# Kernel tuning notes

Measured on AMD Instinct MI355X. Metric: run time of the kernel, lower is better.

The kernel has to match this reference:

```python
import jax, jax.numpy as jnp
import numpy as np

D_MODEL = 2048
N_HEADS = 16
D_K = D_MODEL // N_HEADS
THETA = 10000.0
BATCH = 4
SEQ = 2048


def apply_rope(x, positions, theta=THETA):
    # x: [b, h, s, d], positions: [b, s]
    d = x.shape[-1]
    inv_freq = theta ** (-jnp.arange(0, d, 2, dtype=jnp.float32) / d)  # [d/2]
    ang = positions.astype(jnp.float32)[:, None, :, None] * inv_freq  # [b,1,s,d/2]
    cos, sin = jnp.cos(ang), jnp.sin(ang)
    x1, x2 = x[..., 0::2], x[..., 1::2]
    rot = jnp.stack([x1 * cos - x2 * sin, x1 * sin + x2 * cos], axis=-1)
    return rot.reshape(x.shape).astype(x.dtype)


def setup_inputs() -> dict:
    key = jax.random.key(0)
    ks = jax.random.split(key, 5)
    scale = 1.0 / np.sqrt(D_MODEL)
    return {
        "x": jax.random.normal(ks[0], (BATCH, SEQ, D_MODEL), dtype=jnp.float32),
        "Wq": jax.random.normal(ks[1], (D_MODEL, D_MODEL), dtype=jnp.float32) * scale,
        "Wk": jax.random.normal(ks[2], (D_MODEL, D_MODEL), dtype=jnp.float32) * scale,
        "Wv": jax.random.normal(ks[3], (D_MODEL, D_MODEL), dtype=jnp.float32) * scale,
        "Wo": jax.random.normal(ks[4], (D_MODEL, D_MODEL), dtype=jnp.float32) * scale,
        "token_positions": jnp.broadcast_to(jnp.arange(SEQ, dtype=jnp.int32), (BATCH, SEQ)),
    }


def reference(x, Wq, Wk, Wv, Wo, token_positions):
    b, s, _ = x.shape
    # Linear layers use y = x @ W.T (weight [out, in], no bias)
    q = jnp.einsum('bsd,ed->bse', x, Wq).reshape(b, s, N_HEADS, D_K).transpose(0, 2, 1, 3)
    k = jnp.einsum('bsd,ed->bse', x, Wk).reshape(b, s, N_HEADS, D_K).transpose(0, 2, 1, 3)
    v = jnp.einsum('bsd,ed->bse', x, Wv).reshape(b, s, N_HEADS, D_K).transpose(0, 2, 1, 3)
    q = apply_rope(q, token_positions)
    k = apply_rope(k, token_positions)
    scores = jnp.einsum('bhqd,bhkd->bhqk', q, k) / jnp.sqrt(jnp.float32(D_K))
    causal = jnp.tril(jnp.ones((s, s), dtype=bool))
    scores = jnp.where(causal[None, None], scores, jnp.finfo(scores.dtype).min)
    attn = jax.nn.softmax(scores, axis=-1)
    out = jnp.einsum('bhqk,bhkd->bhqd', attn, v)  # [b,h,s,d]
    out = out.transpose(0, 2, 1, 3).reshape(b, s, D_MODEL)
    return jnp.einsum('bsd,ed->bse', out, Wo)
```

## Files before the change

kernel.cpp:

```cpp
#include <hip/hip_runtime.h>

typedef unsigned int   u32;
typedef unsigned short u16;
typedef float f32x4  __attribute__((ext_vector_type(4)));
typedef float f32x16 __attribute__((ext_vector_type(16)));
typedef short s16x8  __attribute__((ext_vector_type(8)));
typedef u16   u16x4  __attribute__((ext_vector_type(4)));
typedef u16   u16x8  __attribute__((ext_vector_type(8)));
typedef u32   u32x4  __attribute__((ext_vector_type(4)));

#define DEVI __device__ __forceinline__

DEVI u16 f2bf(float f) {
  u32 u = __builtin_bit_cast(u32, f);
  u = (u + 0x7fffu + ((u >> 16) & 1u)) >> 16;
  return (u16)u;
}
DEVI float bf2f(u16 h) { u32 u = (u32)h << 16; return __builtin_bit_cast(float, u); }

DEVI void gload_lds16(const void* g, void* l) {
  __builtin_amdgcn_global_load_lds(
      (const __attribute__((address_space(1))) void*)g,
      (__attribute__((address_space(3))) void*)l, 16, 0, 0);
}

__global__ __launch_bounds__(256)
void convert_kernel(const float* __restrict__ x, const float* __restrict__ Wq,
                    const float* __restrict__ Wk, const float* __restrict__ Wv,
                    const float* __restrict__ Wo, u16* __restrict__ xb, u16* __restrict__ Wb)
{
  const int NX = 1 << 21;
  const int NT = NX + (1 << 21);
  for (int idx = blockIdx.x * 256 + threadIdx.x; idx < NT; idx += gridDim.x * 256) {
    const float* src; u16* dst; size_t off;
    if (idx < NX) { src = x; dst = xb; off = (size_t)idx * 8; }
    else {
      int i2 = idx - NX;
      int wsel = i2 >> 19, r = i2 & ((1 << 19) - 1);
      src = (wsel == 0) ? Wq : (wsel == 1) ? Wk : (wsel == 2) ? Wv : Wo;
      dst = Wb + (size_t)wsel * 4194304;
      off = (size_t)r * 8;
    }
    float4 a = *(const float4*)(src + off), b = *(const float4*)(src + off + 4);
    u16x8 o;
    o[0] = f2bf(a.x); o[1] = f2bf(a.y); o[2] = f2bf(a.z); o[3] = f2bf(a.w);
    o[4] = f2bf(b.x); o[5] = f2bf(b.y); o[6] = f2bf(b.z); o[7] = f2bf(b.w);
    *(u16x8*)(dst + off) = o;
  }
}

template<int EPI, int NBX>
__global__ __launch_bounds__(512, 2)
void gemm256(const u16* __restrict__ Ab, const u16* __restrict__ Bb,
             u16* __restrict__ Qh, u16* __restrict__ Kh, u16* __restrict__ Vt,
             float* __restrict__ Of)
{
  constexpr int K  = 2048;
  constexpr int NTILE = K / 64;
  constexpr int GX = NBX / 4;
  __shared__ __attribute__((aligned(16))) char smem[131072];

  const int t = threadIdx.x;
  const int lane = t & 63, w = t >> 6;
  const int lo = lane & 15, hi = lane >> 4;
  const int wr = w >> 2, wc = w & 3;

  const int nwg = gridDim.x;
  const int cpx = nwg >> 3;
  const int sbid = (blockIdx.x & 7) * cpx + (blockIdx.x >> 3);
  const int g = sbid >> 4, l = sbid & 15;
  const int bx = (g % GX) * 4 + (l & 3);
  const int by = (g / GX) * 4 + (l >> 2);
  const int m0 = by * 256, n0 = bx * 256;

  auto stage = [&](const u16* gbase, char* lds) {
#pragma unroll
    for (int j = 0; j < 4; ++j) {
      int chunk = j * 512 + w * 64 + lane;
      int row = chunk >> 3, cc = chunk & 7;
      const u16* g2 = gbase + (size_t)row * K + ((cc ^ (row & 7)) * 8);
      gload_lds16(g2, lds + (size_t)(j * 512 + w * 64) * 16);
    }
  };

  f32x4 zero = {0.f, 0.f, 0.f, 0.f};
  f32x4 acc[8][4];
#pragma unroll
  for (int i = 0; i < 8; ++i)
#pragma unroll
    for (int j = 0; j < 4; ++j) acc[i][j] = zero;

  const u16* Abase = Ab + (size_t)m0 * K;
  const u16* Bbase = Bb + (size_t)n0 * K;

  stage(Abase + 0 * 64, smem);
  stage(Bbase + 0 * 64, smem + 32768);
  stage(Abase + 1 * 64, smem + 65536);
  stage(Bbase + 1 * 64, smem + 65536 + 32768);

  for (int tt = 0; tt < NTILE; ++tt) {
    if (tt < NTILE - 1) {
      asm volatile("s_waitcnt vmcnt(8)\n\ts_barrier" ::: "memory");
    } else {
      asm volatile("s_waitcnt vmcnt(0)\n\ts_barrier" ::: "memory");
    }
    const char* Alp = smem + (size_t)(tt & 1) * 65536;
    const char* Blp = Alp + 32768;

    s16x8 af0[8], bf0[4];
#pragma unroll
    for (int i = 0; i < 8; ++i) {
      int ra = wr * 128 + i * 16 + lo;
      af0[i] = *(const s16x8*)(Alp + ra * 128 + ((hi * 16) ^ ((ra & 7) << 4)));
    }
#pragma unroll
    for (int j = 0; j < 4; ++j) {
      int rb = wc * 64 + j * 16 + lo;
      bf0[j] = *(const s16x8*)(Blp + rb * 128 + ((hi * 16) ^ ((rb & 7) << 4)));
    }
    __builtin_amdgcn_s_setprio(1);
#pragma unroll
    for (int i = 0; i < 8; ++i)
#pragma unroll
      for (int j = 0; j < 4; ++j)
        acc[i][j] = __builtin_amdgcn_mfma_f32_16x16x32_bf16(af0[i], bf0[j], acc[i][j], 0, 0, 0);
    __builtin_amdgcn_s_setprio(0);

    s16x8 af1[8], bf1[4];
#pragma unroll
    for (int i = 0; i < 8; ++i) {
      int ra = wr * 128 + i * 16 + lo;
      af1[i] = *(const s16x8*)(Alp + ra * 128 + (((4 + hi) * 16) ^ ((ra & 7) << 4)));
    }
#pragma unroll
    for (int j = 0; j < 4; ++j) {
      int rb = wc * 64 + j * 16 + lo;
      bf1[j] = *(const s16x8*)(Blp + rb * 128 + (((4 + hi) * 16) ^ ((rb & 7) << 4)));
    }
    asm volatile("s_waitcnt lgkmcnt(0)\n\ts_barrier" ::: "memory");
    if (tt + 2 < NTILE) {
      char* dst = smem + (size_t)(tt & 1) * 65536;
      stage(Abase + (tt + 2) * 64, dst);
      stage(Bbase + (tt + 2) * 64, dst + 32768);
    }
    __builtin_amdgcn_s_setprio(1);
#pragma unroll
    for (int i = 0; i < 8; ++i)
#pragma unroll
      for (int j = 0; j < 4; ++j)
        acc[i][j] = __builtin_amdgcn_mfma_f32_16x16x32_bf16(af1[i], bf1[j], acc[i][j], 0, 0, 0);
    __builtin_amdgcn_s_setprio(0);
  }

  const int mb = m0 + wr * 128;
  const int nb = n0 + wc * 64;
  if (EPI == 0) {
    const int wsel = n0 >> 11;
    u16* Out = (wsel == 0) ? Qh : (wsel == 1) ? Kh : Vt;
#pragma unroll
    for (int i = 0; i < 8; ++i) {
      int m = mb + i * 16 + hi * 4;
      int b = m >> 11, s0 = m & 2047;
#pragma unroll
      for (int j = 0; j < 4; ++j) {
        int nn = (nb + j * 16 + lo) & 2047;
        int h = nn >> 7, d = nn & 127;
        if (wsel < 2) {
#pragma unroll
          for (int r = 0; r < 4; ++r)
            Out[((size_t)((b * 16 + h) * 2048) + s0 + r) * 128 + d] = f2bf(acc[i][j][r]);
        } else {
          u16x4 v;
#pragma unroll
          for (int r = 0; r < 4; ++r) v[r] = f2bf(acc[i][j][r]);
          *(u16x4*)(Out + ((size_t)(b * 16 + h) * 128 + d) * 2048 + s0) = v;
        }
      }
    }
  } else {
#pragma unroll
    for (int i = 0; i < 8; ++i)
#pragma unroll
      for (int j = 0; j < 4; ++j) {
        int n = nb + j * 16 + lo;
#pragma unroll
        for (int r = 0; r < 4; ++r)
          Of[(size_t)(mb + i * 16 + hi * 4 + r) * 2048 + n] = acc[i][j][r];
      }
  }
}

template<int AM, int WM, int EPI>
__global__ __launch_bounds__(256, 2)
void gemm_nt(const void* __restrict__ Ap, const void* __restrict__ Wp, void* __restrict__ Cp)
{
  constexpr int K = 2048;
  __shared__ __attribute__((aligned(16))) u16 Al[128 * 64];
  __shared__ __attribute__((aligned(16))) u16 Bl[128 * 64];

  const int t = threadIdx.x;
  const int lane = t & 63, w = t >> 6;
  const int lo = lane & 15, hi = lane >> 4;
  const int wm = w >> 1, wn = w & 1;
  const int m0 = blockIdx.y * 128, n0 = blockIdx.x * 128;

  f32x4 zero = {0.f, 0.f, 0.f, 0.f};
  f32x4 acc[4][4];
#pragma unroll
  for (int i = 0; i < 4; ++i)
#pragma unroll
    for (int j = 0; j < 4; ++j) acc[i][j] = zero;

  for (int k0 = 0; k0 < K; k0 += 64) {
    __syncthreads();
    if (AM == 1) {
      const u16* A = (const u16*)Ap;
#pragma unroll
      for (int j = 0; j < 4; ++j) {
        int row = (w * 4 + j) * 8 + (lane >> 3);
        const u16* g = A + (size_t)(m0 + row) * K + k0 + (lane & 7) * 8;
        gload_lds16(g, (char*)Al + (w * 4 + j) * 1024);
      }
    } else {
      const float* A = (const float*)Ap;
#pragma unroll
      for (int c = 0; c < 2; ++c) {
        int chunk = c * 256 + t;
        int row = chunk >> 2, q = chunk & 3;
        const float4* g = reinterpret_cast<const float4*>(A + (size_t)(m0 + row) * K + k0 + q * 16);
        float4 v0 = g[0], v1 = g[1], v2 = g[2], v3 = g[3];
        u16x8 o0, o1;
        o0[0] = f2bf(v0.x); o0[1] = f2bf(v0.y); o0[2] = f2bf(v0.z); o0[3] = f2bf(v0.w);
        o0[4] = f2bf(v1.x); o0[5] = f2bf(v1.y); o0[6] = f2bf(v1.z); o0[7] = f2bf(v1.w);
        o1[0] = f2bf(v2.x); o1[1] = f2bf(v2.y); o1[2] = f2bf(v2.z); o1[3] = f2bf(v2.w);
        o1[4] = f2bf(v3.x); o1[5] = f2bf(v3.y); o1[6] = f2bf(v3.z); o1[7] = f2bf(v3.w);
        int swz = (row & 7) << 4;
        char* base = (char*)Al + row * 128;
        *(u16x8*)(base + ((q * 32)      ^ swz)) = o0;
        *(u16x8*)(base + ((q * 32 + 16) ^ swz)) = o1;
      }
    }
    if (WM == 1) {
      const u16* B = (const u16*)Wp;
#pragma unroll
      for (int j = 0; j < 4; ++j) {
        int row = (w * 4 + j) * 8 + (lane >> 3);
        const u16* g = B + (size_t)(n0 + row) * K + k0 + (lane & 7) * 8;
        gload_lds16(g, (char*)Bl + (w * 4 + j) * 1024);
      }
    } else {
      const float* B = (const float*)Wp;
#pragma unroll
      for (int c = 0; c < 2; ++c) {
        int chunk = c * 256 + t;
        int row = chunk >> 2, q = chunk & 3;
        const float4* g = reinterpret_cast<const float4*>(B + (size_t)(n0 + row) * K + k0 + q * 16);
        float4 v0 = g[0], v1 = g[1], v2 = g[2], v3 = g[3];
        u16x8 o0, o1;
        o0[0] = f2bf(v0.x); o0[1] = f2bf(v0.y); o0[2] = f2bf(v0.z); o0[3] = f2bf(v0.w);
        o0[4] = f2bf(v1.x); o0[5] = f2bf(v1.y); o0[6] = f2bf(v1.z); o0[7] = f2bf(v1.w);
        o1[0] = f2bf(v2.x); o1[1] = f2bf(v2.y); o1[2] = f2bf(v2.z); o1[3] = f2bf(v2.w);
        o1[4] = f2bf(v3.x); o1[5] = f2bf(v3.y); o1[6] = f2bf(v3.z); o1[7] = f2bf(v3.w);
        int swz = (row & 7) << 4;
        char* base = (char*)Bl + row * 128;
        *(u16x8*)(base + ((q * 32)      ^ swz)) = o0;
        *(u16x8*)(base + ((q * 32 + 16) ^ swz)) = o1;
      }
    }
    __syncthreads();
#pragma unroll
    for (int kk = 0; kk < 2; ++kk) {
      s16x8 af[4], bfr[4];
#pragma unroll
      for (int i = 0; i < 4; ++i) {
        int ra = wm * 64 + i * 16 + lo;
        int ca = (kk * 4 + hi) * 16; if (AM != 1) ca ^= (ra & 7) << 4;
        af[i]  = *(const s16x8*)((const char*)Al + ra * 128 + ca);
        int rb = wn * 64 + i * 16 + lo;
        int cb = (kk * 4 + hi) * 16; if (WM != 1) cb ^= (rb & 7) << 4;
        bfr[i] = *(const s16x8*)((const char*)Bl + rb * 128 + cb);
      }
#pragma unroll
      for (int i = 0; i < 4; ++i)
#pragma unroll
        for (int j = 0; j < 4; ++j)
          acc[i][j] = __builtin_amdgcn_mfma_f32_16x16x32_bf16(af[i], bfr[j], acc[i][j], 0, 0, 0);
    }
  }

  const int mb = m0 + wm * 64, nb = n0 + wn * 64;
  if (EPI == 0) {
    u16* Out = (u16*)Cp;
#pragma unroll
    for (int i = 0; i < 4; ++i)
#pragma unroll
      for (int j = 0; j < 4; ++j) {
        int n = nb + j * 16 + lo;
        int h = n >> 7, d = n & 127;
#pragma unroll
        for (int r = 0; r < 4; ++r) {
          int m = mb + i * 16 + hi * 4 + r;
          int b = m >> 11, s = m & 2047;
          Out[((size_t)((b * 16 + h) * 2048 + s)) * 128 + d] = f2bf(acc[i][j][r]);
        }
      }
  } else if (EPI == 1) {
    u16* Out = (u16*)Cp;
#pragma unroll
    for (int i = 0; i < 4; ++i)
#pragma unroll
      for (int j = 0; j < 4; ++j) {
        int n = nb + j * 16 + lo;
        int h = n >> 7, d = n & 127;
        int m = mb + i * 16 + hi * 4;
        int b = m >> 11, s = m & 2047;
        u16x4 v;
#pragma unroll
        for (int r = 0; r < 4; ++r) v[r] = f2bf(acc[i][j][r]);
        *(u16x4*)(Out + ((size_t)((b * 16 + h) * 128 + d)) * 2048 + s) = v;
      }
  } else {
    float* Out = (float*)Cp;
#pragma unroll
    for (int i = 0; i < 4; ++i)
#pragma unroll
      for (int j = 0; j < 4; ++j) {
        int n = nb + j * 16 + lo;
#pragma unroll
        for (int r = 0; r < 4; ++r) {
          int m = mb + i * 16 + hi * 4 + r;
          Out[(size_t)m * 2048 + n] = acc[i][j][r];
        }
      }
  }
}

__global__ __launch_bounds__(256)
void rope_k_kernel(u16* __restrict__ Kh, const int* __restrict__ pos)
{
  const int NP = 4 * 16 * 2048 * 64;
  const float C = -0.20762050593046014f;
  for (int idx = blockIdx.x * 256 + threadIdx.x; idx < NP; idx += gridDim.x * 256) {
    int i = idx & 63;
    int srow = idx >> 6;
    int s = srow & 2047;
    int b = srow >> 15;
    int p = pos[(b << 11) + s];
    float ang = (float)p * exp2f(C * (float)i);
    float sn, cs;
    sincosf(ang, &sn, &cs);
    u32* kp = (u32*)Kh + (size_t)srow * 64 + i;
    u32 v = *kp;
    float x1 = bf2f((u16)(v & 0xffffu)), x2 = bf2f((u16)(v >> 16));
    *kp = (u32)f2bf(x1 * cs - x2 * sn) | ((u32)f2bf(x1 * sn + x2 * cs) << 16);
  }
}

__global__ __launch_bounds__(256, 2)
void attn_kernel(const u16* __restrict__ Qh, const u16* __restrict__ Kh,
                 const u16* __restrict__ Vt, const int* __restrict__ pos,
                 u16* __restrict__ AO)
{
  __shared__ __attribute__((aligned(16))) char smem[65536];

  const int t = threadIdx.x, lane = t & 63, w = t >> 6;
  const int q5 = lane & 31, h5 = lane >> 5;
  const int bid = blockIdx.x;
  const int bh = (((bid >> 3) & 7) << 3) | (bid & 7);
  const int qt = bid >> 6;
  const int qbase = (15 - qt) * 128;
  const int b = bh >> 4;
  const int qrow0 = qbase + w * 32;
  const int q_abs = qrow0 + q5;

  const u16* Kb = Kh + (size_t)bh * 2048 * 128;
  const u16* Vb = Vt + (size_t)bh * 128 * 2048;

  auto stageKV = [&](int kv0, char* dst) {
#pragma unroll
    for (int j = 0; j < 4; ++j) {
      int chunk = j * 256 + w * 64 + lane;
      int row = chunk >> 4, cc = chunk & 15;
      const u16* g = Kb + (size_t)(kv0 + row) * 128 + ((cc ^ (row & 15)) * 8);
      gload_lds16(g, dst + (size_t)chunk * 16);
    }
#pragma unroll
    for (int j = 0; j < 4; ++j) {
      int chunk = j * 256 + w * 64 + lane;
      int pr = chunk >> 4, o16 = chunk & 15;
      int orig = o16 ^ (pr & 15);
      int grow = ((orig >> 3) << 6) + pr;
      const u16* g = Vb + (size_t)grow * 2048 + kv0 + ((orig & 7) * 8);
      gload_lds16(g, dst + 16384 + (size_t)chunk * 16);
    }
  };

  s16x8 qb[8];
  const float CF = -0.20762050593046014f;
  const float QSCALE = 0.08838834764831845f * 1.4426950408889634f;
  {
    float p = (float)pos[(b << 11) + q_abs];
    const u16* qrow = Qh + ((size_t)bh * 2048 + q_abs) * 128;
#pragma unroll
    for (int kb = 0; kb < 8; ++kb) {
      s16x8 raw = *reinterpret_cast<const s16x8*>(qrow + kb * 16 + h5 * 8);
      s16x8 out;
#pragma unroll
      for (int u = 0; u < 4; ++u) {
        float x1 = bf2f((u16)raw[2 * u]), x2 = bf2f((u16)raw[2 * u + 1]);
        float ang = p * exp2f(CF * (float)(kb * 8 + h5 * 4 + u));
        float sn, cs; sincosf(ang, &sn, &cs);
        sn *= QSCALE; cs *= QSCALE;
        out[2 * u]     = (short)f2bf(x1 * cs - x2 * sn);
        out[2 * u + 1] = (short)f2bf(x1 * sn + x2 * cs);
      }
      qb[kb] = out;
    }
  }

  f32x16 o[4];
#pragma unroll
  for (int d = 0; d < 4; ++d)
#pragma unroll
    for (int r = 0; r < 16; ++r) o[d][r] = 0.f;
  float m2 = -1e30f, lp = 0.f;

  const int ntiles = (qbase + 128) >> 6;

  stageKV(0, smem);
  if (ntiles > 1) stageKV(64, smem + 32768);

  for (int tile = 0; tile < ntiles; ++tile) {
    const int kv0 = tile << 6;
    if (tile < ntiles - 1) {
      asm volatile("s_waitcnt vmcnt(8)\n\ts_barrier" ::: "memory");
    } else {
      asm volatile("s_waitcnt vmcnt(0)\n\ts_barrier" ::: "memory");
    }
    const char* Kl = smem + (size_t)(tile & 1) * 32768;
    const char* Vl = Kl + 16384;

    f32x16 st[2];
#pragma unroll
    for (int tt = 0; tt < 2; ++tt)
#pragma unroll
      for (int r = 0; r < 16; ++r) st[tt][r] = 0.f;
    __builtin_amdgcn_s_setprio(1);
#pragma unroll
    for (int tt = 0; tt < 2; ++tt) {
      const char* krow = Kl + (tt * 32 + q5) * 256;
      const int swz = (q5 & 15) << 4;
#pragma unroll
      for (int kb = 0; kb < 8; ++kb) {
        s16x8 ka = *(const s16x8*)(krow + ((kb * 32 + h5 * 16) ^ swz));
        st[tt] = __builtin_amdgcn_mfma_f32_32x32x16_bf16(ka, qb[kb], st[tt], 0, 0, 0);
      }
    }
    __builtin_amdgcn_s_setprio(0);

    const bool needmask = (kv0 + 63 > qrow0);
    float pm = -1e30f;
    if (needmask) {
#pragma unroll
      for (int tt = 0; tt < 2; ++tt)
#pragma unroll
        for (int r = 0; r < 16; ++r) {
          int kvloc = (r & 3) + 8 * (r >> 2) + 4 * h5 + 32 * tt;
          float v = st[tt][r];
          if (kv0 + kvloc > q_abs) v = -1e30f;
          st[tt][r] = v;
          pm = fmaxf(pm, v);
        }
    } else {
#pragma unroll
      for (int tt = 0; tt < 2; ++tt)
#pragma unroll
        for (int r = 0; r < 16; ++r) pm = fmaxf(pm, st[tt][r]);
    }

    if (__any(pm - m2 > 8.0f)) {
      float tm = fmaxf(pm, __shfl_xor(pm, 32));
      float mn = fmaxf(m2, tm);
      float alpha = exp2f(m2 - mn);
      m2 = mn; lp *= alpha;
#pragma unroll
      for (int d = 0; d < 4; ++d)
#pragma unroll
        for (int r = 0; r < 16; ++r) o[d][r] *= alpha;
    }

    s16x8 pb[2][2];
#pragma unroll
    for (int tt = 0; tt < 2; ++tt) {
      u32 pk[8], sw[8];
      float acc = 0.f;
#pragma unroll
      for (int i = 0; i < 8; ++i) {
        float e0 = exp2f(st[tt][2 * i]     - m2);
        float e1 = exp2f(st[tt][2 * i + 1] - m2);
        acc += e0 + e1;
        pk[i] = (u32)f2bf(e0) | ((u32)f2bf(e1) << 16);
      }
      lp += acc;
#pragma unroll
      for (int i = 0; i < 8; ++i)
        sw[i] = (u32)__shfl_xor((int)pk[i], 32);
#pragma unroll
      for (int kv2 = 0; kv2 < 2; ++kv2) {
        int i0 = kv2 * 4;
        u32x4 tmp;
        tmp[0] = h5 ? sw[i0 + 2] : pk[i0];
        tmp[1] = h5 ? sw[i0 + 3] : pk[i0 + 1];
        tmp[2] = h5 ? pk[i0 + 2] : sw[i0];
        tmp[3] = h5 ? pk[i0 + 3] : sw[i0 + 1];
        pb[tt][kv2] = __builtin_bit_cast(s16x8, tmp);
      }
    }

    __builtin_amdgcn_s_setprio(1);
#pragma unroll
    for (int d = 0; d < 4; ++d) {
      const char* vrow = Vl + (((d & 1) * 32 + q5) * 256);
      const int vbase = (d >> 1) * 128;
      const int swz = (q5 & 15) << 4;
#pragma unroll
      for (int tt = 0; tt < 2; ++tt)
#pragma unroll
        for (int kv2 = 0; kv2 < 2; ++kv2) {
          s16x8 va = *(const s16x8*)(vrow + ((vbase + tt * 64 + kv2 * 32 + h5 * 16) ^ swz));
          o[d] = __builtin_amdgcn_mfma_f32_32x32x16_bf16(va, pb[tt][kv2], o[d], 0, 0, 0);
        }
    }
    __builtin_amdgcn_s_setprio(0);

    asm volatile("s_waitcnt lgkmcnt(0)\n\ts_barrier" ::: "memory");
    if (tile + 2 < ntiles)
      stageKV((tile + 2) * 64, smem + (size_t)(tile & 1) * 32768);
  }

  float lt = lp + __shfl_xor(lp, 32);
  float inv = 1.0f / lt;
  __syncthreads();
  char* Olw = smem + w * 8192;
#pragma unroll
  for (int d4 = 0; d4 < 4; ++d4)
#pragma unroll
    for (int r = 0; r < 16; ++r) {
      int dd = d4 * 32 + (r & 3) + 8 * (r >> 2) + 4 * h5;
      *(u16*)(Olw + q5 * 256 + ((dd * 2) ^ ((q5 & 7) << 4))) = f2bf(o[d4][r] * inv);
    }
  __syncthreads();
  const int h = bh & 15;
#pragma unroll
  for (int c = 0; c < 8; ++c) {
    int chunk = c * 256 + t;
    int row = chunk >> 4, sl = chunk & 15;
    u16x8 v = *(const u16x8*)(smem + row * 256 + ((sl * 16) ^ ((row & 7) << 4)));
    *(u16x8*)(AO + ((size_t)(b * 2048 + qbase + row)) * 2048 + h * 128 + sl * 8) = v;
  }
}

extern "C" void kernel_launch(void* const* d_in, const int* in_sizes, int n_in,
                              void* d_out, int out_size, void* d_ws, size_t ws_size,
                              hipStream_t stream)
{
  const float* x  = (const float*)d_in[0];
  const float* Wq = (const float*)d_in[1];
  const float* Wk = (const float*)d_in[2];
  const float* Wv = (const float*)d_in[3];
  const float* Wo = (const float*)d_in[4];
  const int*  pos = (const int*)d_in[5];

  char* ws = (char*)d_ws;
  const size_t MB32 = 33554432;
  u16* Qh = (u16*)(ws);
  u16* Kh = (u16*)(ws + MB32);
  u16* Vt = (u16*)(ws + 2 * MB32);

  dim3 blk(256);

  if (ws_size >= (size_t)167772160) {
    u16* xb = (u16*)(ws + 3 * MB32);
    u16* Wb = (u16*)(ws + 4 * MB32);
    u16* AO = xb;
    convert_kernel<<<2048, blk, 0, stream>>>(x, Wq, Wk, Wv, Wo, xb, Wb);
    gemm256<0, 24><<<768, 512, 0, stream>>>(xb, Wb, Qh, Kh, Vt, nullptr);
    rope_k_kernel<<<2048, blk, 0, stream>>>(Kh, pos);
    attn_kernel<<<1024, blk, 0, stream>>>(Qh, Kh, Vt, pos, AO);
    gemm256<1, 8><<<256, 512, 0, stream>>>(AO, Wb + 3 * 4194304, nullptr, nullptr, nullptr,
                                           (float*)d_out);
  } else {
    u16* AO = (u16*)(ws + 3 * MB32);
    dim3 gg(16, 64);
    gemm_nt<0, 0, 0><<<gg, blk, 0, stream>>>(x, Wq, Qh);
    gemm_nt<0, 0, 0><<<gg, blk, 0, stream>>>(x, Wk, Kh);
    gemm_nt<0, 0, 1><<<gg, blk, 0, stream>>>(x, Wv, Vt);
    rope_k_kernel<<<2048, blk, 0, stream>>>(Kh, pos);
    attn_kernel<<<1024, blk, 0, stream>>>(Qh, Kh, Vt, pos, AO);
    gemm_nt<1, 0, 2><<<gg, blk, 0, stream>>>(AO, Wo, d_out);
  }
}
```

Measured before the change: 440.0 us.

## Fuse K RoPE into QKV GEMM epilogue and remap tile groups

```diff
diff --git a/kernel.cpp b/kernel.cpp
--- a/kernel.cpp
+++ b/kernel.cpp
@@ -53,11 +53,10 @@
 __global__ __launch_bounds__(512, 2)
 void gemm256(const u16* __restrict__ Ab, const u16* __restrict__ Bb,
              u16* __restrict__ Qh, u16* __restrict__ Kh, u16* __restrict__ Vt,
-             float* __restrict__ Of)
+             float* __restrict__ Of, const int* __restrict__ pos)
 {
   constexpr int K  = 2048;
   constexpr int NTILE = K / 64;
-  constexpr int GX = NBX / 4;
   __shared__ __attribute__((aligned(16))) char smem[131072];
 
   const int t = threadIdx.x;
@@ -69,8 +68,17 @@
   const int cpx = nwg >> 3;
   const int sbid = (blockIdx.x & 7) * cpx + (blockIdx.x >> 3);
   const int g = sbid >> 4, l = sbid & 15;
-  const int bx = (g % GX) * 4 + (l & 3);
-  const int by = (g / GX) * 4 + (l >> 2);
+  int gx, gy;
+  if (NBX == 24) {
+    int c3 = g % 3, c2 = (g / 3) & 1, cm = g / 6;
+    gx = (cm & 1) * 3 + c3;
+    gy = (cm >> 1) * 2 + c2;
+  } else {
+    gx = g % (NBX / 4);
+    gy = g / (NBX / 4);
+  }
+  const int bx = gx * 4 + (l & 3);
+  const int by = gy * 4 + (l >> 2);
   const int m0 = by * 256, n0 = bx * 256;
 
   auto stage = [&](const u16* gbase, char* lds) {
@@ -157,6 +165,7 @@
   if (EPI == 0) {
     const int wsel = n0 >> 11;
     u16* Out = (wsel == 0) ? Qh : (wsel == 1) ? Kh : Vt;
+    const float CF = -0.20762050593046014f;
 #pragma unroll
     for (int i = 0; i < 8; ++i) {
       int m = mb + i * 16 + hi * 4;
@@ -165,10 +174,22 @@
       for (int j = 0; j < 4; ++j) {
         int nn = (nb + j * 16 + lo) & 2047;
         int h = nn >> 7, d = nn & 127;
-        if (wsel < 2) {
+        if (wsel == 0) {
 #pragma unroll
           for (int r = 0; r < 4; ++r)
             Out[((size_t)((b * 16 + h) * 2048) + s0 + r) * 128 + d] = f2bf(acc[i][j][r]);
+        } else if (wsel == 1) {
+          float fr = exp2f(CF * (float)(d >> 1));
+#pragma unroll
+          for (int r = 0; r < 4; ++r) {
+            float own = acc[i][j][r];
+            float oth = __shfl_xor(own, 1, 64);
+            float p = (float)pos[(b << 11) + s0 + r];
+            float ang = p * fr;
+            float cs = __cosf(ang), sn = __sinf(ang);
+            float v = (lo & 1) ? (oth * sn + own * cs) : (own * cs - oth * sn);
+            Out[((size_t)((b * 16 + h) * 2048) + s0 + r) * 128 + d] = f2bf(v);
+          }
         } else {
           u16x4 v;
 #pragma unroll
@@ -584,11 +605,10 @@
     u16* Wb = (u16*)(ws + 4 * MB32);
     u16* AO = xb;
     convert_kernel<<<2048, blk, 0, stream>>>(x, Wq, Wk, Wv, Wo, xb, Wb);
-    gemm256<0, 24><<<768, 512, 0, stream>>>(xb, Wb, Qh, Kh, Vt, nullptr);
-    rope_k_kernel<<<2048, blk, 0, stream>>>(Kh, pos);
+    gemm256<0, 24><<<768, 512, 0, stream>>>(xb, Wb, Qh, Kh, Vt, nullptr, pos);
     attn_kernel<<<1024, blk, 0, stream>>>(Qh, Kh, Vt, pos, AO);
     gemm256<1, 8><<<256, 512, 0, stream>>>(AO, Wb + 3 * 4194304, nullptr, nullptr, nullptr,
-                                           (float*)d_out);
+                                           (float*)d_out, pos);
   } else {
     u16* AO = (u16*)(ws + 3 * MB32);
     dim3 gg(16, 64);
```

Measured after the change: 441.0 us. Within noise of the previous version (+0.2%).

## Restructure GEMM main loop into four half-tile phases with interleaved staged loads

Applied to the files above, without the earlier changes.

```diff
diff --git a/kernel.cpp b/kernel.cpp
--- a/kernel.cpp
+++ b/kernel.cpp
@@ -64,6 +64,7 @@
   const int lane = t & 63, w = t >> 6;
   const int lo = lane & 15, hi = lane >> 4;
   const int wr = w >> 2, wc = w & 3;
+  const int swzlo = (lo & 7) << 4;
 
   const int nwg = gridDim.x;
   const int cpx = nwg >> 3;
@@ -73,13 +74,16 @@
   const int by = (g / GX) * 4 + (l >> 2);
   const int m0 = by * 256, n0 = bx * 256;
 
-  auto stage = [&](const u16* gbase, char* lds) {
-#pragma unroll
-    for (int j = 0; j < 4; ++j) {
-      int chunk = j * 512 + w * 64 + lane;
+  const u16* Abase = Ab + (size_t)m0 * K;
+  const u16* Bbase = Bb + (size_t)n0 * K;
+
+  auto stageH = [&](const u16* gbase, char* lds) {
+#pragma unroll
+    for (int jj = 0; jj < 2; ++jj) {
+      int chunk = jj * 512 + t;
       int row = chunk >> 3, cc = chunk & 7;
-      const u16* g2 = gbase + (size_t)row * K + ((cc ^ (row & 7)) * 8);
-      gload_lds16(g2, lds + (size_t)(j * 512 + w * 64) * 16);
+      const u16* gp = gbase + (size_t)row * K + ((cc ^ (row & 7)) * 8);
+      gload_lds16(gp, lds + (size_t)chunk * 16);
     }
   };
 
@@ -90,66 +94,97 @@
 #pragma unroll
     for (int j = 0; j < 4; ++j) acc[i][j] = zero;
 
-  const u16* Abase = Ab + (size_t)m0 * K;
-  const u16* Bbase = Bb + (size_t)n0 * K;
-
-  stage(Abase + 0 * 64, smem);
-  stage(Bbase + 0 * 64, smem + 32768);
-  stage(Abase + 1 * 64, smem + 65536);
-  stage(Bbase + 1 * 64, smem + 65536 + 32768);
-
-  for (int tt = 0; tt < NTILE; ++tt) {
-    if (tt < NTILE - 1) {
-      asm volatile("s_waitcnt vmcnt(8)\n\ts_barrier" ::: "memory");
+  stageH(Abase,                      smem + 0);
+  stageH(Abase + (size_t)128 * K,    smem + 16384);
+  stageH(Bbase,                      smem + 32768);
+  stageH(Bbase + (size_t)128 * K,    smem + 49152);
+  stageH(Bbase + 64,                 smem + 65536 + 32768);
+  asm volatile("s_waitcnt vmcnt(2)\n\ts_barrier" ::: "memory");
+
+  for (int u = 0; u < NTILE; ++u) {
+    char* buf  = smem + (size_t)(u & 1) * 65536;
+    char* obuf = smem + (size_t)((u + 1) & 1) * 65536;
+    const char* Abuf = buf + wr * 16384;
+    const char* Bbuf = buf + 32768 + (wc >> 1) * 16384;
+    const int brow = (wc & 1) * 64;
+
+    s16x8 bk0[4], bk1[4], af[4];
+
+#pragma unroll
+    for (int j = 0; j < 4; ++j)
+      bk0[j] = *(const s16x8*)(Bbuf + (brow + j * 16 + lo) * 128 + ((hi * 16) ^ swzlo));
+#pragma unroll
+    for (int i = 0; i < 4; ++i)
+      af[i] = *(const s16x8*)(Abuf + (i * 16 + lo) * 128 + ((hi * 16) ^ swzlo));
+    if (u + 1 < NTILE)
+      stageH(Bbase + (size_t)(u + 1) * 64 + (size_t)128 * K, obuf + 49152);
+    __builtin_amdgcn_s_barrier();
+    asm volatile("s_waitcnt lgkmcnt(0)" ::: "memory");
+    __builtin_amdgcn_s_setprio(1);
+#pragma unroll
+    for (int i = 0; i < 4; ++i)
+#pragma unroll
+      for (int j = 0; j < 4; ++j)
+        acc[i][j] = __builtin_amdgcn_mfma_f32_16x16x32_bf16(af[i], bk0[j], acc[i][j], 0, 0, 0);
+    __builtin_amdgcn_s_setprio(0);
+    __builtin_amdgcn_s_barrier();
+
+#pragma unroll
+    for (int j = 0; j < 4; ++j)
+      bk1[j] = *(const s16x8*)(Bbuf + (brow + j * 16 + lo) * 128 + (((4 + hi) * 16) ^ swzlo));
+#pragma unroll
+    for (int i = 0; i < 4; ++i)
+      af[i] = *(const s16x8*)(Abuf + (i * 16 + lo) * 128 + (((4 + hi) * 16) ^ swzlo));
+    if (u + 1 < NTILE)
+      stageH(Abase + (size_t)(u + 1) * 64, obuf + 0);
+    __builtin_amdgcn_s_barrier();
+    asm volatile("s_waitcnt lgkmcnt(0)" ::: "memory");
+    __builtin_amdgcn_s_setprio(1);
+#pragma unroll
+    for (int i = 0; i < 4; ++i)
+#pragma unroll
+      for (int j = 0; j < 4; ++j)
+        acc[i][j] = __builtin_amdgcn_mfma_f32_16x16x32_bf16(af[i], bk1[j], acc[i][j], 0, 0, 0);
+    __builtin_amdgcn_s_setprio(0);
+    __builtin_amdgcn_s_barrier();
+
+#pragma unroll
+    for (int i = 0; i < 4; ++i)
+      af[i] = *(const s16x8*)(Abuf + ((4 + i) * 16 + lo) * 128 + ((hi * 16) ^ swzlo));
+    if (u + 1 < NTILE)
+      stageH(Abase + (size_t)(u + 1) * 64 + (size_t)128 * K, obuf + 16384);
+    __builtin_amdgcn_s_barrier();
+    asm volatile("s_waitcnt lgkmcnt(0)" ::: "memory");
+    __builtin_amdgcn_s_setprio(1);
+#pragma unroll
+    for (int i = 0; i < 4; ++i)
+#pragma unroll
+      for (int j = 0; j < 4; ++j)
+        acc[4 + i][j] = __builtin_amdgcn_mfma_f32_16x16x32_bf16(af[i], bk0[j], acc[4 + i][j], 0, 0, 0);
+    __builtin_amdgcn_s_setprio(0);
+    __builtin_amdgcn_s_barrier();
+
+#pragma unroll
+    for (int i = 0; i < 4; ++i)
+      af[i] = *(const s16x8*)(Abuf + ((4 + i) * 16 + lo) * 128 + (((4 + hi) * 16) ^ swzlo));
+    if (u + 2 < NTILE)
+      stageH(Bbase + (size_t)(u + 2) * 64, buf + 32768);
+    __builtin_amdgcn_s_barrier();
+    asm volatile("s_waitcnt lgkmcnt(0)" ::: "memory");
+    __builtin_amdgcn_s_setprio(1);
+#pragma unroll
+    for (int i = 0; i < 4; ++i)
+#pragma unroll
+      for (int j = 0; j < 4; ++j)
+        acc[4 + i][j] = __builtin_amdgcn_mfma_f32_16x16x32_bf16(af[i], bk1[j], acc[4 + i][j], 0, 0, 0);
+    __builtin_amdgcn_s_setprio(0);
+    if (u + 2 < NTILE) {
+      asm volatile("s_waitcnt vmcnt(2)\n\ts_barrier" ::: "memory");
+    } else if (u + 1 < NTILE) {
+      asm volatile("s_waitcnt vmcnt(0)\n\ts_barrier" ::: "memory");
     } else {
-      asm volatile("s_waitcnt vmcnt(0)\n\ts_barrier" ::: "memory");
-    }
-    const char* Alp = smem + (size_t)(tt & 1) * 65536;
-    const char* Blp = Alp + 32768;
-
-    s16x8 af0[8], bf0[4];
-#pragma unroll
-    for (int i = 0; i < 8; ++i) {
-      int ra = wr * 128 + i * 16 + lo;
-      af0[i] = *(const s16x8*)(Alp + ra * 128 + ((hi * 16) ^ ((ra & 7) << 4)));
-    }
-#pragma unroll
-    for (int j = 0; j < 4; ++j) {
-      int rb = wc * 64 + j * 16 + lo;
-      bf0[j] = *(const s16x8*)(Blp + rb * 128 + ((hi * 16) ^ ((rb & 7) << 4)));
-    }
-    __builtin_amdgcn_s_setprio(1);
-#pragma unroll
-    for (int i = 0; i < 8; ++i)
-#pragma unroll
-      for (int j = 0; j < 4; ++j)
-        acc[i][j] = __builtin_amdgcn_mfma_f32_16x16x32_bf16(af0[i], bf0[j], acc[i][j], 0, 0, 0);
-    __builtin_amdgcn_s_setprio(0);
-
-    s16x8 af1[8], bf1[4];
-#pragma unroll
-    for (int i = 0; i < 8; ++i) {
-      int ra = wr * 128 + i * 16 + lo;
-      af1[i] = *(const s16x8*)(Alp + ra * 128 + (((4 + hi) * 16) ^ ((ra & 7) << 4)));
-    }
-#pragma unroll
-    for (int j = 0; j < 4; ++j) {
-      int rb = wc * 64 + j * 16 + lo;
-      bf1[j] = *(const s16x8*)(Blp + rb * 128 + (((4 + hi) * 16) ^ ((rb & 7) << 4)));
-    }
-    asm volatile("s_waitcnt lgkmcnt(0)\n\ts_barrier" ::: "memory");
-    if (tt + 2 < NTILE) {
-      char* dst = smem + (size_t)(tt & 1) * 65536;
-      stage(Abase + (tt + 2) * 64, dst);
-      stage(Bbase + (tt + 2) * 64, dst + 32768);
-    }
-    __builtin_amdgcn_s_setprio(1);
-#pragma unroll
-    for (int i = 0; i < 8; ++i)
-#pragma unroll
-      for (int j = 0; j < 4; ++j)
-        acc[i][j] = __builtin_amdgcn_mfma_f32_16x16x32_bf16(af1[i], bf1[j], acc[i][j], 0, 0, 0);
-    __builtin_amdgcn_s_setprio(0);
+      __builtin_amdgcn_s_barrier();
+    }
   }
 
   const int mb = m0 + wr * 128;
```

After: 447.5 us. Within noise of the previous version (+1.7%).
